# Kernel optimization log

Hardware: AMD Instinct MI355X
Metric: run time of the kernel (lower is better)

## Reference

```python
import jax, jax.numpy as jnp
import numpy as np
import math

STAGE_NUM = 5


def _l2norm(t, axis):
    return t / (1e-6 + jnp.linalg.norm(t, axis=axis, keepdims=True))


def setup_inputs() -> dict:
    key = jax.random.key(0)
    ks = jax.random.split(key, 6)
    b, n, c, h, w, k = 8, 5, 512, 32, 32, 64
    x = jax.random.normal(ks[0], (b, n, c, h, w), dtype=jnp.float32)
    mu = jax.random.normal(ks[1], (1, c, k), dtype=jnp.float32) * math.sqrt(2.0 / k)
    mu = _l2norm(mu, axis=1)
    # 1x1 convs init: normal(0, sqrt(2/(1*1*out_channels)))
    std = math.sqrt(2.0 / c)
    conv1_w = jax.random.normal(ks[2], (c, c), dtype=jnp.float32) * std  # [out,in]
    conv1_b = jnp.zeros((c,), dtype=jnp.float32)
    conv2_w = jax.random.normal(ks[3], (c, c), dtype=jnp.float32) * std
    bn_gamma = jnp.ones((c,), dtype=jnp.float32)
    bn_beta = jnp.zeros((c,), dtype=jnp.float32)
    return {"x": x, "mu": mu, "conv1_w": conv1_w, "conv1_b": conv1_b,
            "conv2_w": conv2_w, "bn_gamma": bn_gamma, "bn_beta": bn_beta}


def reference(x, mu, conv1_w, conv1_b, conv2_w, bn_gamma, bn_beta):
    b, n, c, h, w = x.shape
    xf = x.reshape(b * n, c, h, w)
    idn = xf
    # conv1: 1x1 conv with bias
    y = jnp.einsum('bchw,dc->bdhw', xf, conv1_w) + conv1_b[None, :, None, None]
    # [b, c, N] with N = n*h*w
    y = y.reshape(b, n, c, h, w).transpose(0, 2, 1, 3, 4).reshape(b, c, n * h * w)
    mu_b = jnp.broadcast_to(mu, (b, c, mu.shape[2]))
    z = None
    # EM iterations (no_grad in original; fwd-only so just compute)
    for _ in range(STAGE_NUM):
        z = jax.nn.softmax(jnp.einsum('bcn,bck->bnk', y, mu_b), axis=2)  # [b,N,k]
        z_ = z / (1e-6 + z.sum(axis=1, keepdims=True))
        mu_b = _l2norm(jnp.einsum('bcn,bnk->bck', y, z_), axis=1)
    # reconstruction: mu @ z^T -> [b,c,N]
    rec = jnp.einsum('bck,bnk->bcn', mu_b, z)
    rec = jax.nn.relu(rec.reshape(b, c, n, h, w))
    rec = rec.transpose(0, 2, 1, 3, 4).reshape(b * n, c, h, w)
    # conv2 (no bias) + BatchNorm (training-mode batch stats)
    y2 = jnp.einsum('bchw,dc->bdhw', rec, conv2_w)
    mean = y2.mean(axis=(0, 2, 3), keepdims=True)
    var = y2.var(axis=(0, 2, 3), keepdims=True)
    y2 = (y2 - mean) * jax.lax.rsqrt(var + 1e-5)
    y2 = y2 * bn_gamma[None, :, None, None] + bn_beta[None, :, None, None]
    out = jax.nn.relu(y2 + idn).reshape(b, n, c, h, w)
    return out, mu_b
```

## Files before the change

### kernel.cpp

```cpp
#include <hip/hip_runtime.h>
#include <math.h>

#define CH 512
#define K 64
#define BB 8
#define NIMG 5
#define HW 1024
#define NP 5120
#define BI 40

typedef __attribute__((ext_vector_type(8))) _Float16 f16x8;
typedef __attribute__((ext_vector_type(4))) _Float16 f16x4;
typedef __attribute__((ext_vector_type(4))) float f32x4;
typedef __attribute__((ext_vector_type(8))) short s16x8;

#define AS1 __attribute__((address_space(1)))
#define AS3 __attribute__((address_space(3)))

__device__ inline long mufrag_idx(int b, int c, int k) {
    int cc = c >> 5, l4 = (c >> 3) & 3, e = c & 7;
    int j = k >> 4, l15 = k & 15;
    int lane = l4 * 16 + l15;
    return ((long)b << 15) + (((cc * 4 + j) * 64 + lane) << 3) + e;
}

__global__ __launch_bounds__(256) void wconv(const float* __restrict__ w,
                                             _Float16* __restrict__ o)
{
    int i = blockIdx.x * 256 + threadIdx.x;
    o[i] = (_Float16)w[i];
}

__global__ __launch_bounds__(256) void transpose_f16(
    const float* __restrict__ in, _Float16* __restrict__ out, int P)
{
    __shared__ float tile[64][65];
    int t = threadIdx.x;
    int p0 = blockIdx.x * 64, c0 = blockIdx.y * 64;
    long ibase = (long)blockIdx.z * CH * P;
    long obase = (long)blockIdx.z * P * CH;
    int pl = t & 63, chh = t >> 6;
    #pragma unroll
    for (int i = 0; i < 16; ++i)
        tile[chh + i * 4][pl] = in[ibase + (long)(c0 + chh + i * 4) * P + p0 + pl];
    __syncthreads();
    int cc = t & 31, pr = t >> 5;
    #pragma unroll
    for (int i = 0; i < 8; ++i) {
        int p = pr + i * 8;
        _Float16 lo = (_Float16)tile[cc * 2][p];
        _Float16 hi = (_Float16)tile[cc * 2 + 1][p];
        unsigned lob = (unsigned)*(unsigned short*)&lo;
        unsigned hib = (unsigned)*(unsigned short*)&hi;
        *(unsigned*)&out[obase + (long)(p0 + p) * CH + c0 + cc * 2] = lob | (hib << 16);
    }
}

__global__ __launch_bounds__(256) void bcast_mu2(const float* __restrict__ mu_in,
                                                 float* __restrict__ mu_cur,
                                                 _Float16* __restrict__ muF)
{
    int i = blockIdx.x * 256 + threadIdx.x;
    float v = mu_in[i & 32767];
    mu_cur[i] = v;
    int b = i >> 15, ck = i & 32767, c = ck >> 6, k = ck & 63;
    muF[mufrag_idx(b, c, k)] = (_Float16)v;
}

__global__ __launch_bounds__(256) void conv_tile(
    const _Float16* __restrict__ Wh, const _Float16* __restrict__ inT,
    const float* __restrict__ bias, float* __restrict__ y2,
    _Float16* __restrict__ y16, _Float16* __restrict__ yT16,
    float* __restrict__ stats, float* __restrict__ statsq, int mode)
{
    __shared__ _Float16 Wt[128 * 64];
    __shared__ _Float16 Xt[128 * 64];
    int t = threadIdx.x;
    int lane = t & 63, w = t >> 6;
    int l15 = lane & 15, l4 = lane >> 4;
    int wd = w & 1, wp = w >> 1;
    int bi = blockIdx.z;
    int d0 = blockIdx.y * 128;
    int pl0 = blockIdx.x * 128;
    long prow0 = (long)bi * HW + pl0;
    int ci_row = lane >> 3;
    int colb_phys = (lane & 7) * 16;

    f32x4 acc[4][4];
    #pragma unroll
    for (int ai = 0; ai < 4; ++ai)
        #pragma unroll
        for (int bj = 0; bj < 4; ++bj) acc[ai][bj] = (f32x4){0.f, 0.f, 0.f, 0.f};

    for (int c0 = 0; c0 < CH; c0 += 64) {
        __syncthreads();
        #pragma unroll
        for (int i = 0; i < 4; ++i) {
            int row = w * 32 + i * 8 + ci_row;
            int cb = colb_phys ^ ((row & 7) << 4);
            const _Float16* srcW = Wh + (long)(d0 + row) * CH + c0 + (cb >> 1);
            const _Float16* srcX = inT + (prow0 + row) * (long)CH + c0 + (cb >> 1);
            __builtin_amdgcn_global_load_lds((const AS1 void*)srcW,
                (AS3 void*)&Wt[(w * 32 + i * 8) * 64], 16, 0, 0);
            __builtin_amdgcn_global_load_lds((const AS1 void*)srcX,
                (AS3 void*)&Xt[(w * 32 + i * 8) * 64], 16, 0, 0);
        }
        __syncthreads();
        #pragma unroll
        for (int kk = 0; kk < 2; ++kk) {
            f16x8 af[4], bf[4];
            #pragma unroll
            for (int ai = 0; ai < 4; ++ai) {
                int row = wd * 64 + ai * 16 + l15;
                int cb = (kk * 64 + l4 * 16) ^ ((row & 7) << 4);
                af[ai] = *(const f16x8*)((const char*)Wt + row * 128 + cb);
            }
            #pragma unroll
            for (int bj = 0; bj < 4; ++bj) {
                int row = wp * 64 + bj * 16 + l15;
                int cb = (kk * 64 + l4 * 16) ^ ((row & 7) << 4);
                bf[bj] = *(const f16x8*)((const char*)Xt + row * 128 + cb);
            }
            #pragma unroll
            for (int ai = 0; ai < 4; ++ai)
                #pragma unroll
                for (int bj = 0; bj < 4; ++bj)
                    acc[ai][bj] = __builtin_amdgcn_mfma_f32_16x16x32_f16(
                        af[ai], bf[bj], acc[ai][bj], 0, 0, 0);
        }
    }

    int b = bi / NIMG, n = bi % NIMG;
    if (mode == 0) {
        #pragma unroll
        for (int ai = 0; ai < 4; ++ai) {
            int dd = d0 + wd * 64 + ai * 16 + l4 * 4;
            float b0 = bias[dd], b1 = bias[dd + 1], b2 = bias[dd + 2], b3 = bias[dd + 3];
            #pragma unroll
            for (int bj = 0; bj < 4; ++bj) {
                int pb = n * HW + pl0 + wp * 64 + bj * 16 + l15;
                f16x4 pk = { (_Float16)(acc[ai][bj][0] + b0), (_Float16)(acc[ai][bj][1] + b1),
                             (_Float16)(acc[ai][bj][2] + b2), (_Float16)(acc[ai][bj][3] + b3) };
                *(f16x4*)&yT16[((long)b * NP + pb) * CH + dd] = pk;
                long yb = ((long)b * CH + dd) * NP + pb;
                y16[yb] = pk[0];
                y16[yb + NP] = pk[1];
                y16[yb + 2 * NP] = pk[2];
                y16[yb + 3 * NP] = pk[3];
            }
        }
    } else {
        long obase = (long)bi * CH * HW;
        #pragma unroll
        for (int ai = 0; ai < 4; ++ai) {
            int dd = d0 + wd * 64 + ai * 16 + l4 * 4;
            #pragma unroll
            for (int bj = 0; bj < 4; ++bj) {
                int p = pl0 + wp * 64 + bj * 16 + l15;
                long o = obase + (long)dd * HW + p;
                y2[o] = acc[ai][bj][0];
                y2[o + HW] = acc[ai][bj][1];
                y2[o + 2 * HW] = acc[ai][bj][2];
                y2[o + 3 * HW] = acc[ai][bj][3];
            }
        }
        #pragma unroll
        for (int ai = 0; ai < 4; ++ai) {
            #pragma unroll
            for (int i = 0; i < 4; ++i) {
                float s = acc[ai][0][i] + acc[ai][1][i] + acc[ai][2][i] + acc[ai][3][i];
                float q = acc[ai][0][i] * acc[ai][0][i] + acc[ai][1][i] * acc[ai][1][i]
                        + acc[ai][2][i] * acc[ai][2][i] + acc[ai][3][i] * acc[ai][3][i];
                #pragma unroll
                for (int off = 1; off < 16; off <<= 1) {
                    s += __shfl_xor(s, off, 64);
                    q += __shfl_xor(q, off, 64);
                }
                if (l15 == 0) {
                    int dd = d0 + wd * 64 + ai * 16 + l4 * 4 + i;
                    atomicAdd(&stats[dd], s);
                    atomicAdd(&statsq[dd], q);
                }
            }
        }
    }
}

__global__ __launch_bounds__(256) void stage_z_mfma(
    const _Float16* __restrict__ yT, const _Float16* __restrict__ muF,
    _Float16* __restrict__ zT, _Float16* __restrict__ z16,
    float* __restrict__ zsum, int writeZ)
{
    __shared__ float zred[256];
    int t = threadIdx.x;
    int w = t >> 6, lane = t & 63, l15 = lane & 15, l4 = lane >> 4;
    int p0 = blockIdx.x * 128 + w * 32;
    int b = blockIdx.y;
    const _Float16* mf = muF + ((long)b << 15);
    const _Float16* a0p = yT + ((long)b * NP + p0 + l15) * CH + l4 * 8;
    const _Float16* a1p = yT + ((long)b * NP + p0 + 16 + l15) * CH + l4 * 8;
    f32x4 acc[2][4];
    #pragma unroll
    for (int pb = 0; pb < 2; ++pb)
        #pragma unroll
        for (int j = 0; j < 4; ++j) acc[pb][j] = (f32x4){0.f, 0.f, 0.f, 0.f};
    #pragma unroll
    for (int cc = 0; cc < 16; ++cc) {
        f16x8 a0 = *(const f16x8*)(a0p + cc * 32);
        f16x8 a1 = *(const f16x8*)(a1p + cc * 32);
        #pragma unroll
        for (int j = 0; j < 4; ++j) {
            f16x8 bj = *(const f16x8*)&mf[(((cc * 4 + j) * 64) + lane) * 8];
            acc[0][j] = __builtin_amdgcn_mfma_f32_16x16x32_f16(a0, bj, acc[0][j], 0, 0, 0);
            acc[1][j] = __builtin_amdgcn_mfma_f32_16x16x32_f16(a1, bj, acc[1][j], 0, 0, 0);
        }
    }
    long ztbase = (long)b * K * NP;
    long zbase = (long)b * NP * K;
    float part[4] = {0.f, 0.f, 0.f, 0.f};
    #pragma unroll
    for (int pb = 0; pb < 2; ++pb) {
        float zv[4][4];
        #pragma unroll
        for (int i = 0; i < 4; ++i) {
            float m = fmaxf(fmaxf(acc[pb][0][i], acc[pb][1][i]),
                            fmaxf(acc[pb][2][i], acc[pb][3][i]));
            #pragma unroll
            for (int off = 1; off < 16; off <<= 1) m = fmaxf(m, __shfl_xor(m, off, 64));
            float e0 = __expf(acc[pb][0][i] - m);
            float e1 = __expf(acc[pb][1][i] - m);
            float e2 = __expf(acc[pb][2][i] - m);
            float e3 = __expf(acc[pb][3][i] - m);
            float s = e0 + e1 + e2 + e3;
            #pragma unroll
            for (int off = 1; off < 16; off <<= 1) s += __shfl_xor(s, off, 64);
            float inv = 1.f / s;
            zv[0][i] = e0 * inv; zv[1][i] = e1 * inv;
            zv[2][i] = e2 * inv; zv[3][i] = e3 * inv;
        }
        int prow = p0 + pb * 16 + l4 * 4;
        #pragma unroll
        for (int j = 0; j < 4; ++j) {
            f16x4 pk = { (_Float16)zv[j][0], (_Float16)zv[j][1],
                         (_Float16)zv[j][2], (_Float16)zv[j][3] };
            *(f16x4*)&zT[ztbase + (long)(l15 + 16 * j) * NP + prow] = pk;
        }
        if (writeZ) {
            #pragma unroll
            for (int j = 0; j < 4; ++j)
                #pragma unroll
                for (int i = 0; i < 4; ++i)
                    z16[zbase + (long)(prow + i) * K + l15 + 16 * j] = (_Float16)zv[j][i];
        }
        #pragma unroll
        for (int j = 0; j < 4; ++j)
            part[j] += zv[j][0] + zv[j][1] + zv[j][2] + zv[j][3];
    }
    #pragma unroll
    for (int j = 0; j < 4; ++j) {
        part[j] += __shfl_xor(part[j], 16, 64);
        part[j] += __shfl_xor(part[j], 32, 64);
    }
    if (l4 == 0) {
        #pragma unroll
        for (int j = 0; j < 4; ++j) zred[w * 64 + l15 + 16 * j] = part[j];
    }
    __syncthreads();
    if (t < 64)
        atomicAdd(&zsum[b * 64 + t], zred[t] + zred[64 + t] + zred[128 + t] + zred[192 + t]);
}

__global__ __launch_bounds__(256) void stage_mu_mfma(
    const _Float16* __restrict__ y16, const _Float16* __restrict__ zT,
    float* __restrict__ macc)
{
    int t = threadIdx.x;
    int w = t >> 6, lane = t & 63, l15 = lane & 15, l4 = lane >> 4;
    int pc = blockIdx.x, ct = blockIdx.y, b = blockIdx.z;
    int c0 = ct * 128 + w * 32;
    int pbase = pc * 640;
    const _Float16* zrow = zT + (long)b * K * NP + (long)l15 * NP + l4 * 8;
    const _Float16* a0p = y16 + ((long)b * CH + c0 + l15) * NP + l4 * 8;
    const _Float16* a1p = y16 + ((long)b * CH + c0 + 16 + l15) * NP + l4 * 8;
    f32x4 acc[2][4];
    #pragma unroll
    for (int ci = 0; ci < 2; ++ci)
        #pragma unroll
        for (int j = 0; j < 4; ++j) acc[ci][j] = (f32x4){0.f, 0.f, 0.f, 0.f};
    for (int p0 = pbase; p0 < pbase + 640; p0 += 32) {
        f16x8 a0 = *(const f16x8*)(a0p + p0);
        f16x8 a1 = *(const f16x8*)(a1p + p0);
        #pragma unroll
        for (int j = 0; j < 4; ++j) {
            f16x8 bj = *(const f16x8*)(zrow + (long)(16 * j) * NP + p0);
            acc[0][j] = __builtin_amdgcn_mfma_f32_16x16x32_f16(a0, bj, acc[0][j], 0, 0, 0);
            acc[1][j] = __builtin_amdgcn_mfma_f32_16x16x32_f16(a1, bj, acc[1][j], 0, 0, 0);
        }
    }
    float* mp = macc + ((long)pc * BB + b) * K * CH;
    #pragma unroll
    for (int ci = 0; ci < 2; ++ci)
        #pragma unroll
        for (int j = 0; j < 4; ++j)
            *(f32x4*)&mp[(long)(l15 + 16 * j) * CH + c0 + ci * 16 + l4 * 4] = acc[ci][j];
}

__global__ __launch_bounds__(256) void mu_norm2(
    const float* __restrict__ macc, const float* __restrict__ zsum,
    float* __restrict__ mu_cur, _Float16* __restrict__ mu16,
    _Float16* __restrict__ muF)
{
    int gw = blockIdx.x * 4 + (threadIdx.x >> 6);
    int lane = threadIdx.x & 63;
    int b = gw >> 6, k = gw & 63;
    float v[8];
    float s = 0.f;
    #pragma unroll
    for (int ci = 0; ci < 8; ++ci) {
        int c = ci * 64 + lane;
        float a = 0.f;
        #pragma unroll
        for (int pcc = 0; pcc < 8; ++pcc)
            a += macc[(((long)pcc * BB + b) * K + k) * CH + c];
        v[ci] = a; s += a * a;
    }
    #pragma unroll
    for (int off = 1; off < 64; off <<= 1) s += __shfl_xor(s, off, 64);
    float d = 1e-6f + zsum[b * 64 + k];
    float scale = 1.f / (1e-6f * d + sqrtf(s));
    long mb = (long)b << 15;
    #pragma unroll
    for (int ci = 0; ci < 8; ++ci) {
        int c = ci * 64 + lane;
        float m = v[ci] * scale;
        mu_cur[mb + (long)c * K + k] = m;
        mu16[mb + (long)c * K + k] = (_Float16)m;
        muF[mufrag_idx(b, c, k)] = (_Float16)m;
    }
}

__global__ __launch_bounds__(256) void rec_mfma(
    const _Float16* __restrict__ z16, const _Float16* __restrict__ mu16,
    _Float16* __restrict__ recT)
{
    __shared__ _Float16 rt[64 * 80];
    int t = threadIdx.x;
    int w = t >> 6, lane = t & 63, l15 = lane & 15, l4 = lane >> 4;
    int p0 = blockIdx.x * 64, ct = blockIdx.y, b = blockIdx.z;
    const _Float16* zb = z16 + (long)b * NP * K;
    const _Float16* mb = mu16 + ((long)b << 15) + (long)(ct * 64 + w * 16 + l15) * K + l4 * 8;
    f32x4 acc[4];
    #pragma unroll
    for (int pj = 0; pj < 4; ++pj) acc[pj] = (f32x4){0.f, 0.f, 0.f, 0.f};
    #pragma unroll
    for (int kc = 0; kc < 64; kc += 32) {
        f16x8 bfr = *(const f16x8*)(mb + kc);
        #pragma unroll
        for (int pj = 0; pj < 4; ++pj) {
            f16x8 a = *(const f16x8*)(zb + (long)(p0 + pj * 16 + l15) * K + kc + l4 * 8);
            acc[pj] = __builtin_amdgcn_mfma_f32_16x16x32_f16(a, bfr, acc[pj], 0, 0, 0);
        }
    }
    #pragma unroll
    for (int pj = 0; pj < 4; ++pj)
        #pragma unroll
        for (int i = 0; i < 4; ++i)
            rt[(pj * 16 + l4 * 4 + i) * 80 + w * 16 + l15] = (_Float16)fmaxf(acc[pj][i], 0.f);
    __syncthreads();
    #pragma unroll
    for (int it = 0; it < 2; ++it) {
        int l = t + it * 256;
        int row = l >> 3, s8 = l & 7;
        *(s16x8*)&recT[((long)b * NP + p0 + row) * CH + ct * 64 + s8 * 8] =
            *(const s16x8*)&rt[row * 80 + s8 * 8];
    }
}

__global__ __launch_bounds__(256) void final_kernel(
    const float* __restrict__ y2, const float* __restrict__ x,
    const float* __restrict__ stats, const float* __restrict__ statsq,
    const float* __restrict__ gamma, const float* __restrict__ beta,
    const float* __restrict__ mu_cur, float* __restrict__ out)
{
    long i4 = (long)blockIdx.x * 256 + threadIdx.x;
    const long NMAIN4 = (long)BI * CH * HW / 4;
    if (i4 < NMAIN4) {
        long i = i4 * 4;
        int d = (int)((i >> 10) & (CH - 1));
        float s = stats[d], sq = statsq[d];
        const float inv = 1.f / (float)(BI * HW);
        float mean = s * inv;
        float var = sq * inv - mean * mean;
        float rs = rsqrtf(var + 1e-5f);
        float g = rs * gamma[d];
        float bb = beta[d] - mean * g;
        float4 yv = *(const float4*)&y2[i];
        float4 xv = *(const float4*)&x[i];
        float4 ov;
        ov.x = fmaxf(yv.x * g + bb + xv.x, 0.f);
        ov.y = fmaxf(yv.y * g + bb + xv.y, 0.f);
        ov.z = fmaxf(yv.z * g + bb + xv.z, 0.f);
        ov.w = fmaxf(yv.w * g + bb + xv.w, 0.f);
        *(float4*)&out[i] = ov;
    } else {
        long j = (i4 - NMAIN4) * 4;
        *(float4*)&out[(long)BI * CH * HW + j] = *(const float4*)&mu_cur[j];
    }
}

extern "C" void kernel_launch(void* const* d_in, const int* in_sizes, int n_in,
                              void* d_out, int out_size, void* d_ws, size_t ws_size,
                              hipStream_t stream) {
    const float* x   = (const float*)d_in[0];
    const float* mu0 = (const float*)d_in[1];
    const float* w1  = (const float*)d_in[2];
    const float* b1  = (const float*)d_in[3];
    const float* w2  = (const float*)d_in[4];
    const float* gm  = (const float*)d_in[5];
    const float* bt  = (const float*)d_in[6];
    float* out = (float*)d_out;

    float* ws = (float*)d_ws;
    _Float16* y16h  = (_Float16*)(ws);
    _Float16* yT16h = (_Float16*)(ws + 10485760);
    _Float16* xTh   = (_Float16*)(ws + 20971520);
    _Float16* zTh   = (_Float16*)(ws + 20971520);
    _Float16* z16h  = (_Float16*)(ws + 22282240);
    float*    macc  = ws + 23592960;
    float*    mu_cur = ws + 31457280;
    _Float16* Wh1   = (_Float16*)(ws + 31719424);
    _Float16* Wh2   = (_Float16*)(ws + 31850496);
    _Float16* mu16h = (_Float16*)(ws + 31981568);
    _Float16* muFh  = (_Float16*)(ws + 32112640);
    float*    zsum  = ws + 32243712;
    float*    stats = ws + 32246272;
    float*    statsq = ws + 32246784;
    float* y2 = out;

    hipMemsetAsync(zsum, 0, 3584 * sizeof(float), stream);

    wconv<<<1024, 256, 0, stream>>>(w1, Wh1);
    wconv<<<1024, 256, 0, stream>>>(w2, Wh2);
    transpose_f16<<<dim3(16, 8, 40), 256, 0, stream>>>(x, xTh, HW);
    conv_tile<<<dim3(8, 4, 40), 256, 0, stream>>>(Wh1, xTh, b1, nullptr, y16h, yT16h,
                                                  nullptr, nullptr, 0);
    bcast_mu2<<<1024, 256, 0, stream>>>(mu0, mu_cur, muFh);

    for (int s = 0; s < 5; ++s) {
        stage_z_mfma<<<dim3(40, 8), 256, 0, stream>>>(yT16h, muFh, zTh, z16h,
                                                      zsum + s * 512, s == 4);
        stage_mu_mfma<<<dim3(8, 4, 8), 256, 0, stream>>>(y16h, zTh, macc);
        mu_norm2<<<128, 256, 0, stream>>>(macc, zsum + s * 512, mu_cur, mu16h, muFh);
    }

    rec_mfma<<<dim3(80, 8, 8), 256, 0, stream>>>(z16h, mu16h, yT16h);
    conv_tile<<<dim3(8, 4, 40), 256, 0, stream>>>(Wh2, yT16h, nullptr, y2, nullptr, nullptr,
                                                  stats, statsq, 1);
    long total4 = ((long)BI * CH * HW + (long)BB * CH * K) / 4;
    final_kernel<<<(int)((total4 + 255) / 256), 256, 0, stream>>>(
        y2, x, stats, statsq, gm, bt, mu_cur, out);
}
```

Measured before the change: 469.9 us.

## Split BN stats into separate kernel and raise EM stage parallelism

```diff
diff --git a/kernel.cpp b/kernel.cpp
--- a/kernel.cpp
+++ b/kernel.cpp
@@ -70,8 +70,7 @@
 __global__ __launch_bounds__(256) void conv_tile(
     const _Float16* __restrict__ Wh, const _Float16* __restrict__ inT,
     const float* __restrict__ bias, float* __restrict__ y2,
-    _Float16* __restrict__ y16, _Float16* __restrict__ yT16,
-    float* __restrict__ stats, float* __restrict__ statsq, int mode)
+    _Float16* __restrict__ y16, _Float16* __restrict__ yT16, int mode)
 {
     __shared__ _Float16 Wt[128 * 64];
     __shared__ _Float16 Xt[128 * 64];
@@ -164,25 +163,34 @@
                 y2[o + 3 * HW] = acc[ai][bj][3];
             }
         }
-        #pragma unroll
-        for (int ai = 0; ai < 4; ++ai) {
-            #pragma unroll
-            for (int i = 0; i < 4; ++i) {
-                float s = acc[ai][0][i] + acc[ai][1][i] + acc[ai][2][i] + acc[ai][3][i];
-                float q = acc[ai][0][i] * acc[ai][0][i] + acc[ai][1][i] * acc[ai][1][i]
-                        + acc[ai][2][i] * acc[ai][2][i] + acc[ai][3][i] * acc[ai][3][i];
-                #pragma unroll
-                for (int off = 1; off < 16; off <<= 1) {
-                    s += __shfl_xor(s, off, 64);
-                    q += __shfl_xor(q, off, 64);
-                }
-                if (l15 == 0) {
-                    int dd = d0 + wd * 64 + ai * 16 + l4 * 4 + i;
-                    atomicAdd(&stats[dd], s);
-                    atomicAdd(&statsq[dd], q);
-                }
-            }
-        }
+    }
+}
+
+__global__ __launch_bounds__(256) void bn_stats2(const float* __restrict__ y2,
+                                                 float* __restrict__ stats,
+                                                 float* __restrict__ statsq)
+{
+    int d = blockIdx.x;
+    int t = threadIdx.x;
+    float s = 0.f, q = 0.f;
+    for (int bi = 0; bi < BI; ++bi) {
+        const float* p = y2 + (long)bi * CH * HW + (long)d * HW;
+        float4 v = *(const float4*)&p[t * 4];
+        s += v.x + v.y + v.z + v.w;
+        q += v.x * v.x + v.y * v.y + v.z * v.z + v.w * v.w;
+    }
+    #pragma unroll
+    for (int off = 1; off < 64; off <<= 1) {
+        s += __shfl_xor(s, off, 64);
+        q += __shfl_xor(q, off, 64);
+    }
+    __shared__ float ps[8];
+    int wv = t >> 6, ln = t & 63;
+    if (ln == 0) { ps[wv] = s; ps[4 + wv] = q; }
+    __syncthreads();
+    if (t == 0) {
+        stats[d]  = ps[0] + ps[1] + ps[2] + ps[3];
+        statsq[d] = ps[4] + ps[5] + ps[6] + ps[7];
     }
 }
 
@@ -194,70 +202,59 @@
     __shared__ float zred[256];
     int t = threadIdx.x;
     int w = t >> 6, lane = t & 63, l15 = lane & 15, l4 = lane >> 4;
-    int p0 = blockIdx.x * 128 + w * 32;
+    int p0 = blockIdx.x * 64 + w * 16;
     int b = blockIdx.y;
     const _Float16* mf = muF + ((long)b << 15);
     const _Float16* a0p = yT + ((long)b * NP + p0 + l15) * CH + l4 * 8;
-    const _Float16* a1p = yT + ((long)b * NP + p0 + 16 + l15) * CH + l4 * 8;
-    f32x4 acc[2][4];
-    #pragma unroll
-    for (int pb = 0; pb < 2; ++pb)
-        #pragma unroll
-        for (int j = 0; j < 4; ++j) acc[pb][j] = (f32x4){0.f, 0.f, 0.f, 0.f};
+    f32x4 acc[4];
+    #pragma unroll
+    for (int j = 0; j < 4; ++j) acc[j] = (f32x4){0.f, 0.f, 0.f, 0.f};
     #pragma unroll
     for (int cc = 0; cc < 16; ++cc) {
         f16x8 a0 = *(const f16x8*)(a0p + cc * 32);
-        f16x8 a1 = *(const f16x8*)(a1p + cc * 32);
         #pragma unroll
         for (int j = 0; j < 4; ++j) {
             f16x8 bj = *(const f16x8*)&mf[(((cc * 4 + j) * 64) + lane) * 8];
-            acc[0][j] = __builtin_amdgcn_mfma_f32_16x16x32_f16(a0, bj, acc[0][j], 0, 0, 0);
-            acc[1][j] = __builtin_amdgcn_mfma_f32_16x16x32_f16(a1, bj, acc[1][j], 0, 0, 0);
-        }
-    }
+            acc[j] = __builtin_amdgcn_mfma_f32_16x16x32_f16(a0, bj, acc[j], 0, 0, 0);
+        }
+    }
+    float zv[4][4];
+    #pragma unroll
+    for (int i = 0; i < 4; ++i) {
+        float m = fmaxf(fmaxf(acc[0][i], acc[1][i]), fmaxf(acc[2][i], acc[3][i]));
+        #pragma unroll
+        for (int off = 1; off < 16; off <<= 1) m = fmaxf(m, __shfl_xor(m, off, 64));
+        float e0 = __expf(acc[0][i] - m);
+        float e1 = __expf(acc[1][i] - m);
+        float e2 = __expf(acc[2][i] - m);
+        float e3 = __expf(acc[3][i] - m);
+        float s = e0 + e1 + e2 + e3;
+        #pragma unroll
+        for (int off = 1; off < 16; off <<= 1) s += __shfl_xor(s, off, 64);
+        float inv = 1.f / s;
+        zv[0][i] = e0 * inv; zv[1][i] = e1 * inv;
+        zv[2][i] = e2 * inv; zv[3][i] = e3 * inv;
+    }
+    int prow = p0 + l4 * 4;
     long ztbase = (long)b * K * NP;
-    long zbase = (long)b * NP * K;
-    float part[4] = {0.f, 0.f, 0.f, 0.f};
-    #pragma unroll
-    for (int pb = 0; pb < 2; ++pb) {
-        float zv[4][4];
-        #pragma unroll
-        for (int i = 0; i < 4; ++i) {
-            float m = fmaxf(fmaxf(acc[pb][0][i], acc[pb][1][i]),
-                            fmaxf(acc[pb][2][i], acc[pb][3][i]));
-            #pragma unroll
-            for (int off = 1; off < 16; off <<= 1) m = fmaxf(m, __shfl_xor(m, off, 64));
-            float e0 = __expf(acc[pb][0][i] - m);
-            float e1 = __expf(acc[pb][1][i] - m);
-            float e2 = __expf(acc[pb][2][i] - m);
-            float e3 = __expf(acc[pb][3][i] - m);
-            float s = e0 + e1 + e2 + e3;
-            #pragma unroll
-            for (int off = 1; off < 16; off <<= 1) s += __shfl_xor(s, off, 64);
-            float inv = 1.f / s;
-            zv[0][i] = e0 * inv; zv[1][i] = e1 * inv;
-            zv[2][i] = e2 * inv; zv[3][i] = e3 * inv;
-        }
-        int prow = p0 + pb * 16 + l4 * 4;
-        #pragma unroll
-        for (int j = 0; j < 4; ++j) {
-            f16x4 pk = { (_Float16)zv[j][0], (_Float16)zv[j][1],
-                         (_Float16)zv[j][2], (_Float16)zv[j][3] };
-            *(f16x4*)&zT[ztbase + (long)(l15 + 16 * j) * NP + prow] = pk;
-        }
-        if (writeZ) {
-            #pragma unroll
-            for (int j = 0; j < 4; ++j)
-                #pragma unroll
-                for (int i = 0; i < 4; ++i)
-                    z16[zbase + (long)(prow + i) * K + l15 + 16 * j] = (_Float16)zv[j][i];
-        }
+    #pragma unroll
+    for (int j = 0; j < 4; ++j) {
+        f16x4 pk = { (_Float16)zv[j][0], (_Float16)zv[j][1],
+                     (_Float16)zv[j][2], (_Float16)zv[j][3] };
+        *(f16x4*)&zT[ztbase + (long)(l15 + 16 * j) * NP + prow] = pk;
+    }
+    if (writeZ) {
+        long zbase = (long)b * NP * K;
         #pragma unroll
         for (int j = 0; j < 4; ++j)
-            part[j] += zv[j][0] + zv[j][1] + zv[j][2] + zv[j][3];
-    }
+            #pragma unroll
+            for (int i = 0; i < 4; ++i)
+                z16[zbase + (long)(prow + i) * K + l15 + 16 * j] = (_Float16)zv[j][i];
+    }
+    float part[4];
     #pragma unroll
     for (int j = 0; j < 4; ++j) {
+        part[j] = zv[j][0] + zv[j][1] + zv[j][2] + zv[j][3];
         part[j] += __shfl_xor(part[j], 16, 64);
         part[j] += __shfl_xor(part[j], 32, 64);
     }
@@ -278,7 +275,7 @@
     int w = t >> 6, lane = t & 63, l15 = lane & 15, l4 = lane >> 4;
     int pc = blockIdx.x, ct = blockIdx.y, b = blockIdx.z;
     int c0 = ct * 128 + w * 32;
-    int pbase = pc * 640;
+    int pbase = pc * 320;
     const _Float16* zrow = zT + (long)b * K * NP + (long)l15 * NP + l4 * 8;
     const _Float16* a0p = y16 + ((long)b * CH + c0 + l15) * NP + l4 * 8;
     const _Float16* a1p = y16 + ((long)b * CH + c0 + 16 + l15) * NP + l4 * 8;
@@ -287,7 +284,7 @@
     for (int ci = 0; ci < 2; ++ci)
         #pragma unroll
         for (int j = 0; j < 4; ++j) acc[ci][j] = (f32x4){0.f, 0.f, 0.f, 0.f};
-    for (int p0 = pbase; p0 < pbase + 640; p0 += 32) {
+    for (int p0 = pbase; p0 < pbase + 320; p0 += 32) {
         f16x8 a0 = *(const f16x8*)(a0p + p0);
         f16x8 a1 = *(const f16x8*)(a1p + p0);
         #pragma unroll
@@ -320,7 +317,7 @@
         int c = ci * 64 + lane;
         float a = 0.f;
         #pragma unroll
-        for (int pcc = 0; pcc < 8; ++pcc)
+        for (int pcc = 0; pcc < 16; ++pcc)
             a += macc[(((long)pcc * BB + b) * K + k) * CH + c];
         v[ci] = a; s += a * a;
     }
@@ -437,25 +434,24 @@
     float*    statsq = ws + 32246784;
     float* y2 = out;
 
-    hipMemsetAsync(zsum, 0, 3584 * sizeof(float), stream);
+    hipMemsetAsync(zsum, 0, 2560 * sizeof(float), stream);
 
     wconv<<<1024, 256, 0, stream>>>(w1, Wh1);
     wconv<<<1024, 256, 0, stream>>>(w2, Wh2);
     transpose_f16<<<dim3(16, 8, 40), 256, 0, stream>>>(x, xTh, HW);
-    conv_tile<<<dim3(8, 4, 40), 256, 0, stream>>>(Wh1, xTh, b1, nullptr, y16h, yT16h,
-                                                  nullptr, nullptr, 0);
+    conv_tile<<<dim3(8, 4, 40), 256, 0, stream>>>(Wh1, xTh, b1, nullptr, y16h, yT16h, 0);
     bcast_mu2<<<1024, 256, 0, stream>>>(mu0, mu_cur, muFh);
 
     for (int s = 0; s < 5; ++s) {
-        stage_z_mfma<<<dim3(40, 8), 256, 0, stream>>>(yT16h, muFh, zTh, z16h,
+        stage_z_mfma<<<dim3(80, 8), 256, 0, stream>>>(yT16h, muFh, zTh, z16h,
                                                       zsum + s * 512, s == 4);
-        stage_mu_mfma<<<dim3(8, 4, 8), 256, 0, stream>>>(y16h, zTh, macc);
+        stage_mu_mfma<<<dim3(16, 4, 8), 256, 0, stream>>>(y16h, zTh, macc);
         mu_norm2<<<128, 256, 0, stream>>>(macc, zsum + s * 512, mu_cur, mu16h, muFh);
     }
 
     rec_mfma<<<dim3(80, 8, 8), 256, 0, stream>>>(z16h, mu16h, yT16h);
-    conv_tile<<<dim3(8, 4, 40), 256, 0, stream>>>(Wh2, yT16h, nullptr, y2, nullptr, nullptr,
-                                                  stats, statsq, 1);
+    conv_tile<<<dim3(8, 4, 40), 256, 0, stream>>>(Wh2, yT16h, nullptr, y2, nullptr, nullptr, 1);
+    bn_stats2<<<512, 256, 0, stream>>>(y2, stats, statsq);
     long total4 = ((long)BI * CH * HW + (long)BB * CH * K) / 4;
     final_kernel<<<(int)((total4 + 255) / 256), 256, 0, stream>>>(
         y2, x, stats, statsq, gm, bt, mu_cur, out);
```

Result: faster. 426.3 us (-9.3%).
